# Performance work log

Hardware: AMD Instinct MI355X
Metric: run time of the kernel (lower is better)

The kernel has to match this reference:

```python
import jax, jax.numpy as jnp
import numpy as np

N = 20000
E = 320000
C = 16   # in_channels
G = 8    # growth_channels
H = 16   # kernel MLP hidden = RDB in_channels
DIM = 3
OMEGA = 100.0
BETA = 0.2


def _u(k, shape, s):
    return jax.random.uniform(k, shape, jnp.float32, -s, s)


def setup_inputs() -> dict:
    key = jax.random.key(0)
    ks = jax.random.split(key, 64)
    x = jax.random.normal(ks[0], (N, C), jnp.float32)
    pos = jax.random.normal(ks[1], (N, DIM), jnp.float32)
    # random edges with no self loops (add_remaining_self_loops appends them in reference)
    src = jax.random.randint(ks[2], (E,), 0, N)
    off = jax.random.randint(ks[3], (E,), 1, N)
    dst = (src + off) % N
    edge_index = jnp.stack([src, dst])
    d = {"x": x, "edge_index": edge_index, "pos": pos}
    ins = [C, C + G, C + 2 * G]
    outs = [G, G, C]
    i = 4
    for ci, (cin, cout) in enumerate(zip(ins, outs), 1):
        # SineLayer weights: uniform(-1/in_features, 1/in_features); biases ~ torch Linear default
        d[f"c{ci}_w0"] = _u(ks[i], (H, DIM + 1), 1.0 / (DIM + 1)); i += 1
        d[f"c{ci}_b0"] = _u(ks[i], (H,), 1.0 / np.sqrt(DIM + 1)); i += 1
        d[f"c{ci}_w1"] = _u(ks[i], (H, H), 1.0 / H); i += 1
        d[f"c{ci}_b1"] = _u(ks[i], (H,), 1.0 / np.sqrt(H)); i += 1
        d[f"c{ci}_w2"] = _u(ks[i], (H, H), 1.0 / H); i += 1
        d[f"c{ci}_b2"] = _u(ks[i], (H,), 1.0 / np.sqrt(H)); i += 1
        # final Linear(hidden -> in_size), stored transposed as [in_size, hidden]
        d[f"c{ci}_wl"] = _u(ks[i], (cin, H), 1.0 / np.sqrt(H)); i += 1
        d[f"c{ci}_bl"] = _u(ks[i], (cin,), 1.0 / np.sqrt(H)); i += 1
        d[f"c{ci}_bias"] = jnp.zeros((1, cout), jnp.float32); i += 1
    return d


def _edge_feat(pos, src, dst):
    # rel_pos = pos[dst] - pos[src]; spherical (rho, theta/pi, phi/pi), NaN at rho=0 -> 0
    rel = pos[dst] - pos[src]                              # [E,3]
    sq = jnp.sum(rel * rel, axis=1)
    zero = sq <= 0.0                                       # self loops
    rho = jnp.where(zero, 0.0, jnp.sqrt(jnp.where(zero, 1.0, sq)))
    theta = jnp.arctan2(jnp.where(zero, 0.0, rel[:, 1]), jnp.where(zero, 1.0, rel[:, 0]))
    phi = jnp.arcsin(jnp.clip(jnp.where(zero, 0.0, rel[:, 2]) / jnp.where(zero, 1.0, rho), -1.0, 1.0))
    return jnp.stack([rho, theta / jnp.pi, phi / jnp.pi], axis=1)  # [E,3]


def _gconv(feat, x, src, dst, n, out_ch, w0, b0, w1, b1, w2, b2, wl, bl, bias):
    # vectorized over output channels: channel index c is the 4th input of sin0
    base = feat @ w0[:, :3].T + b0                          # [E,H]
    ch = jnp.arange(out_ch, dtype=feat.dtype)               # [O]
    h = jnp.sin(OMEGA * (base[:, None, :] + ch[None, :, None] * w0[:, 3]))   # [E,O,H]
    h = jnp.sin(OMEGA * (jnp.einsum('eoh,gh->eog', h, w1) + b1))
    h = jnp.sin(OMEGA * (jnp.einsum('eoh,gh->eog', h, w2) + b2))
    xj = x[src]                                             # [E,in]
    # msg[e,o] = (Wl h[e,o] + bl) . x_j[e]  ==  h[e,o] . (Wl^T x_j[e]) + bl . x_j[e]
    msg = jnp.einsum('eoh,eh->eo', h, xj @ wl) + (xj @ bl)[:, None]
    return jax.ops.segment_sum(msg, dst, num_segments=n) + bias


def reference(x, edge_index, pos,
              c1_w0, c1_b0, c1_w1, c1_b1, c1_w2, c1_b2, c1_wl, c1_bl, c1_bias,
              c2_w0, c2_b0, c2_w1, c2_b1, c2_w2, c2_b2, c2_wl, c2_bl, c2_bias,
              c3_w0, c3_b0, c3_w1, c3_b1, c3_w2, c3_b2, c3_wl, c3_bl, c3_bias):
    n = x.shape[0]
    loop = jnp.arange(n, dtype=edge_index.dtype)
    src = jnp.concatenate([edge_index[0], loop])
    dst = jnp.concatenate([edge_index[1], loop])
    feat = _edge_feat(pos, src, dst)
    x1 = jax.nn.selu(_gconv(feat, x, src, dst, n, G, c1_w0, c1_b0, c1_w1, c1_b1, c1_w2, c1_b2, c1_wl, c1_bl, c1_bias))
    x2 = jax.nn.selu(_gconv(feat, jnp.concatenate([x, x1], 1), src, dst, n, G, c2_w0, c2_b0, c2_w1, c2_b1, c2_w2, c2_b2, c2_wl, c2_bl, c2_bias))
    x3 = jax.nn.selu(_gconv(feat, jnp.concatenate([x, x1, x2], 1), src, dst, n, C, c3_w0, c3_b0, c3_w1, c3_b1, c3_w2, c3_b2, c3_wl, c3_bl, c3_bias))
    return x + BETA * x3
```

## Files before the change

kernel.cpp:

```cpp
#include <hip/hip_runtime.h>
#include <math.h>

#define N_NODES 20000
#define N_EDGES 320000
#define HID 16
#define OMEGA 100.0f
#define BETA 0.2f
#define REVC 0.15915494309189535f

#define OFF_W0I 0
#define OFF_B1  64
#define OFF_B2  80
#define OFF_A2  128
#define OFF_WLH 384
#define OFF_WLL 640
#define OFF_AO  896
#define OFF_H2V 9088
#define P_SIZE  9472

typedef float  f32x4 __attribute__((ext_vector_type(4)));
typedef short  s16x8 __attribute__((ext_vector_type(8)));

__device__ __forceinline__ float sinrev(float x) { return __builtin_amdgcn_sinf(x); }
__device__ __forceinline__ float cosrev(float x) { return __builtin_amdgcn_cosf(x); }
__device__ __forceinline__ float fract_f(float x) { return __builtin_amdgcn_fractf(x); }

__device__ __forceinline__ float selu_f(float v) {
    const float a  = 1.6732632423543772f;
    const float sc = 1.0507009873554805f;
    return sc * (v > 0.f ? v : a * expm1f(v));
}

__device__ __forceinline__ f32x4 mfma16(s16x8 a, s16x8 b, f32x4 c) {
    return __builtin_amdgcn_mfma_f32_16x16x32_bf16(a, b, c, 0, 0, 0);
}

__device__ __forceinline__ unsigned pk_hi(float a, float b) {
    return (__float_as_uint(b) & 0xFFFF0000u) | (__float_as_uint(a) >> 16);
}
__device__ __forceinline__ float lo_of(float a) {
    return a - __uint_as_float(__float_as_uint(a) & 0xFFFF0000u);
}

union U4 { uint4 v; s16x8 s; };

struct PrepArgs {
    const float* w0[3]; const float* b0[3]; const float* w1[3]; const float* b1[3];
    const float* w2[3]; const float* b2[3]; const float* wl[3];
    float* P[3];
};

__global__ __launch_bounds__(256) void prep_kernel(PrepArgs A)
{
    const int INS[3]  = {16, 24, 32};
    const int OUTS[3] = {8, 8, 16};
    int c = blockIdx.x;
    int IN = INS[c], OUT = OUTS[c];
    const float* w0 = A.w0[c]; const float* b0 = A.b0[c];
    const float* w1 = A.w1[c]; const float* b1 = A.b1[c];
    const float* w2 = A.w2[c]; const float* b2 = A.b2[c];
    const float* wl = A.wl[c];
    float* P = A.P[c];
    unsigned* Pu = (unsigned*)P;

    __shared__ float W1s[256], W2s[256], cosB[256], sinB[256], w0c[16];
    int t = threadIdx.x;
    const float s = OMEGA * REVC;
    W1s[t] = s * w1[t];
    W2s[t] = s * w2[t];
    if (t < 16) w0c[t] = s * w0[t * 4 + 3];
    __syncthreads();

    if (t < 64) { int h = t >> 2, k = t & 3; P[t] = (k < 3) ? s * w0[h * 4 + k] : s * b0[h]; }
    if (t >= 64 && t < 80)  P[t] = s * b1[t - 64];
    if (t >= 80 && t < 96)  P[t] = s * b2[t - 80];

    if (t < OUT * 16) {
        int o = t >> 4, h = t & 15;
        float ang = fract_f((float)o * w0c[h]);
        cosB[t] = cosrev(ang);
        sinB[t] = sinrev(ang);
    }
    __syncthreads();

    if (t < 64) {
        int g = t & 15, q = t >> 4;
        float w[4], l[4];
#pragma unroll
        for (int j = 0; j < 4; j++) { w[j] = W2s[g * 16 + 4 * q + j]; l[j] = lo_of(w[j]); }
        ((uint4*)(Pu + OFF_A2))[t] = make_uint4(pk_hi(w[0], w[1]), pk_hi(w[2], w[3]),
                                                pk_hi(l[0], l[1]), pk_hi(l[2], l[3]));
    }
    if (t >= 64 && t < 128) {
        int lane = t - 64, g = lane & 15, q = lane >> 4;
        float v[8], l[8];
#pragma unroll
        for (int e = 0; e < 8; e++) {
            int i = 8 * q + e;
            v[e] = (i < IN) ? wl[i * 16 + g] : 0.f;
            l[e] = lo_of(v[e]);
        }
        ((uint4*)(Pu + OFF_WLH))[lane] = make_uint4(pk_hi(v[0], v[1]), pk_hi(v[2], v[3]),
                                                    pk_hi(v[4], v[5]), pk_hi(v[6], v[7]));
        ((uint4*)(Pu + OFF_WLL))[lane] = make_uint4(pk_hi(l[0], l[1]), pk_hi(l[2], l[3]),
                                                    pk_hi(l[4], l[5]), pk_hi(l[6], l[7]));
    }
    for (int idx = t; idx < OUT * 64; idx += 256) {
        int o = idx >> 6, lane = idx & 63, g = lane & 15, q = lane >> 4;
        float v[8], l[8];
#pragma unroll
        for (int e = 0; e < 8; e++) {
            int k = 8 * q + e;
            float a = (k < 16) ? W1s[g * 16 + k] * cosB[o * 16 + k]
                               : W1s[g * 16 + (k - 16)] * sinB[o * 16 + (k - 16)];
            v[e] = a; l[e] = lo_of(a);
        }
        ((uint4*)(Pu + OFF_AO + o * 512))[lane] =
            make_uint4(pk_hi(v[0], v[1]), pk_hi(v[2], v[3]), pk_hi(v[4], v[5]), pk_hi(v[6], v[7]));
        ((uint4*)(Pu + OFF_AO + o * 512 + 256))[lane] =
            make_uint4(pk_hi(l[0], l[1]), pk_hi(l[2], l[3]), pk_hi(l[4], l[5]), pk_hi(l[6], l[7]));
    }
    if (t < OUT) {
        float oc = (float)t;
        float h0[HID], h1[HID];
#pragma unroll
        for (int h = 0; h < HID; h++)
            h0[h] = sinrev(fract_f(fmaf(oc, w0c[h], s * b0[h])));
#pragma unroll
        for (int g = 0; g < HID; g++) {
            float sa = s * b1[g];
#pragma unroll
            for (int h = 0; h < HID; h++) sa += h0[h] * W1s[g * HID + h];
            h1[g] = sinrev(sa);
        }
#pragma unroll
        for (int g = 0; g < HID; g++) {
            float sa = s * b2[g];
#pragma unroll
            for (int h = 0; h < HID; h++) sa += h1[h] * W2s[g * HID + h];
            P[OFF_H2V + t * HID + g] = sinrev(sa);
        }
    }
}

__global__ __launch_bounds__(256) void fused_pre_kernel(
    const int* __restrict__ ei, const float* __restrict__ pos,
    const float* __restrict__ x,
    float4* __restrict__ feat, float* __restrict__ xcat,
    const float* __restrict__ wl1, const float* __restrict__ bl1,
    float* __restrict__ tb, float* __restrict__ blxb)
{
    int b = blockIdx.x;
    if (b < 1250) {
        int e = b * 256 + threadIdx.x;
        if (e >= N_EDGES) return;
        int s = ei[e], d = ei[N_EDGES + e];
        float rx = pos[d * 3 + 0] - pos[s * 3 + 0];
        float ry = pos[d * 3 + 1] - pos[s * 3 + 1];
        float rz = pos[d * 3 + 2] - pos[s * 3 + 2];
        float sq = rx * rx + ry * ry + rz * rz;
        float4 f = make_float4(0.f, 0.f, 0.f, 0.f);
        if (sq > 0.f) {
            float rho = sqrtf(sq);
            float th  = atan2f(ry, rx);
            float ph  = asinf(fminf(fmaxf(rz / rho, -1.f), 1.f));
            const float inv_pi = 0.31830988618379067f;
            f = make_float4(rho, th * inv_pi, ph * inv_pi, 0.f);
        }
        feat[e] = f;
    } else if (b < 2500) {
        int i = (b - 1250) * 256 + threadIdx.x;
        if (i >= N_NODES * 16) return;
        int n = i >> 4, cc = i & 15;
        xcat[n * 32 + cc] = x[i];
    } else {
        int n = (b - 2500) * 256 + threadIdx.x;
        if (n >= N_NODES) return;
        float tn[HID];
#pragma unroll
        for (int h = 0; h < HID; h++) tn[h] = 0.f;
        float bx = 0.f;
#pragma unroll
        for (int i = 0; i < 16; i++) {
            float xi = x[n * 16 + i];
            bx += bl1[i] * xi;
#pragma unroll
            for (int h = 0; h < HID; h++) tn[h] += wl1[i * 16 + h] * xi;
        }
#pragma unroll
        for (int h = 0; h < HID; h++) tb[n * 16 + h] = tn[h];
        blxb[n] = bx;
    }
}

template<int OUT, int IN>
__global__ __launch_bounds__(256) void conv_kernel(
    const int* __restrict__ ei, const float4* __restrict__ feat,
    const float* __restrict__ xcat, const float* __restrict__ P,
    const float* __restrict__ bl, float* __restrict__ acc)
{
    constexpr int L2O = (OUT == 16) ? 4 : 3;
    constexpr int EPI = 64 / OUT;
    constexpr int NI  = 16 / EPI;

    __shared__ float sm[4][OUT * 4 * 17];
    const unsigned* Pu = (const unsigned*)P;
    int wslot = threadIdx.x >> 6;
    int wid  = (blockIdx.x * 256 + threadIdx.x) >> 6;
    int lane = threadIdx.x & 63;
    int e16 = lane & 15, q = lane >> 4;
    int e = wid * 16 + e16;
    int src = ei[e];
    int dst = ei[N_EDGES + e];
    float4 f = feat[e];

    float tr[8];
    {
        const float4* w0i = (const float4*)P;
        int hb = (q & 1) * 8;
#pragma unroll
        for (int j = 0; j < 8; j++) {
            float4 w = w0i[hb + j];
            float ang = fract_f(w.w + f.x * w.x + f.y * w.y + f.z * w.z);
            tr[j] = (q < 2) ? sinrev(ang) : cosrev(ang);
        }
    }
    U4 Bh, Bl;
    Bh.v = make_uint4(pk_hi(tr[0], tr[1]), pk_hi(tr[2], tr[3]),
                      pk_hi(tr[4], tr[5]), pk_hi(tr[6], tr[7]));
    Bl.v = make_uint4(pk_hi(lo_of(tr[0]), lo_of(tr[1])), pk_hi(lo_of(tr[2]), lo_of(tr[3])),
                      pk_hi(lo_of(tr[4]), lo_of(tr[5])), pk_hi(lo_of(tr[6]), lo_of(tr[7])));

    float xv[8];
#pragma unroll
    for (int j = 0; j < 8; j++) xv[j] = 0.f;
    if (8 * q < IN) {
        const f32x4* xr = (const f32x4*)(xcat + src * 32 + 8 * q);
        f32x4 x0 = xr[0], x1 = xr[1];
        xv[0] = x0[0]; xv[1] = x0[1]; xv[2] = x0[2]; xv[3] = x0[3];
        xv[4] = x1[0]; xv[5] = x1[1]; xv[6] = x1[2]; xv[7] = x1[3];
    }
    U4 Xh, Xl;
    Xh.v = make_uint4(pk_hi(xv[0], xv[1]), pk_hi(xv[2], xv[3]),
                      pk_hi(xv[4], xv[5]), pk_hi(xv[6], xv[7]));
    Xl.v = make_uint4(pk_hi(lo_of(xv[0]), lo_of(xv[1])), pk_hi(lo_of(xv[2]), lo_of(xv[3])),
                      pk_hi(lo_of(xv[4]), lo_of(xv[5])), pk_hi(lo_of(xv[6]), lo_of(xv[7])));
    U4 WLh, WLl;
    WLh.v = ((const uint4*)(Pu + OFF_WLH))[lane];
    WLl.v = ((const uint4*)(Pu + OFF_WLL))[lane];
    f32x4 T = {0.f, 0.f, 0.f, 0.f};
    T = mfma16(WLh.s, Xh.s, T);
    T = mfma16(WLh.s, Xl.s, T);
    T = mfma16(WLl.s, Xh.s, T);

    float bx = 0.f;
    if (8 * q < IN) {
        const f32x4* blr = (const f32x4*)(bl + 8 * q);
        f32x4 b0v = blr[0], b1v = blr[1];
        bx = b0v[0] * xv[0] + b0v[1] * xv[1] + b0v[2] * xv[2] + b0v[3] * xv[3]
           + b1v[0] * xv[4] + b1v[1] * xv[5] + b1v[2] * xv[6] + b1v[3] * xv[7];
    }
    bx += __shfl_xor(bx, 16);
    bx += __shfl_xor(bx, 32);

    U4 A2; A2.v = ((const uint4*)(Pu + OFF_A2))[lane];
    f32x4 c1 = *(const f32x4*)(P + OFF_B1 + 4 * q);
    f32x4 c2 = *(const f32x4*)(P + OFF_B2 + 4 * q);

#pragma unroll 2
    for (int o = 0; o < OUT; ++o) {
        U4 Ah, Al;
        Ah.v = ((const uint4*)(Pu + OFF_AO + o * 512))[lane];
        Al.v = ((const uint4*)(Pu + OFF_AO + o * 512 + 256))[lane];
        f32x4 D = c1;
        D = mfma16(Ah.s, Bh.s, D);
        D = mfma16(Ah.s, Bl.s, D);
        D = mfma16(Al.s, Bh.s, D);
        float h1[4];
#pragma unroll
        for (int j = 0; j < 4; j++) h1[j] = sinrev(D[j]);
        unsigned p0 = pk_hi(h1[0], h1[1]), p1 = pk_hi(h1[2], h1[3]);
        unsigned l0 = pk_hi(lo_of(h1[0]), lo_of(h1[1])), l1 = pk_hi(lo_of(h1[2]), lo_of(h1[3]));
        U4 Ph, Pl;
        Ph.v = make_uint4(p0, p1, p0, p1);
        Pl.v = make_uint4(l0, l1, l0, l1);
        f32x4 D2 = c2;
        D2 = mfma16(A2.s, Ph.s, D2);
        D2 = mfma16(A2.s, Pl.s, D2);
        float p = sinrev(D2[0]) * T[0] + sinrev(D2[1]) * T[1]
                + sinrev(D2[2]) * T[2] + sinrev(D2[3]) * T[3];
        if (q == 0) p += bx;
        sm[wslot][(o * 4 + q) * 17 + e16] = p;
    }

    int oo = lane & (OUT - 1);
    int el = lane >> L2O;
#pragma unroll
    for (int j = 0; j < NI; j++) {
        int ej = j * EPI + el;
        int dj = __shfl(dst, ej);
        float v = sm[wslot][(oo * 4 + 0) * 17 + ej] + sm[wslot][(oo * 4 + 1) * 17 + ej]
                + sm[wslot][(oo * 4 + 2) * 17 + ej] + sm[wslot][(oo * 4 + 3) * 17 + ej];
        atomicAdd(&acc[dj * OUT + oo], v);
    }
}

template<int OUT, int CO>
__global__ __launch_bounds__(256) void finish_mid_kernel(
    const float* __restrict__ acc, const float* __restrict__ bias,
    const float* __restrict__ h2v,
    float* __restrict__ tb, float* __restrict__ blxb,
    float* __restrict__ xcat,
    const float* __restrict__ wlN, const float* __restrict__ blN)
{
    int n = blockIdx.x * 256 + threadIdx.x;
    if (n >= N_NODES) return;
    float trr[HID];
#pragma unroll
    for (int h = 0; h < HID; h++) trr[h] = tb[n * 16 + h];
    float bx = blxb[n];
    float xrow[CO + OUT];
#pragma unroll
    for (int i = 0; i < CO; i++) xrow[i] = xcat[n * 32 + i];
#pragma unroll
    for (int o = 0; o < OUT; o++) {
        float m = bx;
#pragma unroll
        for (int h = 0; h < HID; h++) m += h2v[o * 16 + h] * trr[h];
        float v = selu_f(acc[n * OUT + o] + bias[o] + m);
        xrow[CO + o] = v;
        xcat[n * 32 + CO + o] = v;
    }
    float tn[HID];
#pragma unroll
    for (int h = 0; h < HID; h++) tn[h] = 0.f;
    float bxn = 0.f;
#pragma unroll
    for (int i = 0; i < CO + OUT; i++) {
        float xi = xrow[i];
        bxn += blN[i] * xi;
#pragma unroll
        for (int h = 0; h < HID; h++) tn[h] += wlN[i * 16 + h] * xi;
    }
#pragma unroll
    for (int h = 0; h < HID; h++) tb[n * 16 + h] = tn[h];
    blxb[n] = bxn;
}

__global__ __launch_bounds__(256) void finish_out_kernel(
    const float* __restrict__ acc, const float* __restrict__ bias,
    const float* __restrict__ h2v,
    const float* __restrict__ tb, const float* __restrict__ blxb,
    const float* __restrict__ x, float* __restrict__ out)
{
    int n = blockIdx.x * 256 + threadIdx.x;
    if (n >= N_NODES) return;
    float trr[HID];
#pragma unroll
    for (int h = 0; h < HID; h++) trr[h] = tb[n * 16 + h];
    float bx = blxb[n];
#pragma unroll
    for (int c = 0; c < 16; c++) {
        float m = bx;
#pragma unroll
        for (int h = 0; h < HID; h++) m += h2v[c * 16 + h] * trr[h];
        out[n * 16 + c] = x[n * 16 + c] + BETA * selu_f(acc[n * 16 + c] + bias[c] + m);
    }
}

extern "C" void kernel_launch(void* const* d_in, const int* in_sizes, int n_in,
                              void* d_out, int out_size, void* d_ws, size_t ws_size,
                              hipStream_t stream)
{
    const float* x   = (const float*)d_in[0];
    const int*   ei  = (const int*)d_in[1];
    const float* pos = (const float*)d_in[2];

    const float* W[27];
    for (int i = 0; i < 27; i++) W[i] = (const float*)d_in[3 + i];

    float* ws    = (float*)d_ws;
    float4* feat = (float4*)ws;
    float* xcat  = ws + (size_t)N_EDGES * 4;
    float* acc1  = xcat + (size_t)N_NODES * 32;
    float* acc2  = acc1 + (size_t)N_NODES * 8;
    float* acc3  = acc2 + (size_t)N_NODES * 8;
    float* P1    = acc3 + (size_t)N_NODES * 16;
    float* P2    = P1 + P_SIZE;
    float* P3    = P2 + P_SIZE;
    float* tb    = P3 + P_SIZE;
    float* blxb  = tb + (size_t)N_NODES * 16;
    float* out   = (float*)d_out;

    hipMemsetAsync(acc1, 0, (size_t)N_NODES * 32 * sizeof(float), stream);

    PrepArgs pa;
    for (int c = 0; c < 3; c++) {
        pa.w0[c] = W[9 * c + 0]; pa.b0[c] = W[9 * c + 1];
        pa.w1[c] = W[9 * c + 2]; pa.b1[c] = W[9 * c + 3];
        pa.w2[c] = W[9 * c + 4]; pa.b2[c] = W[9 * c + 5];
        pa.wl[c] = W[9 * c + 6];
    }
    pa.P[0] = P1; pa.P[1] = P2; pa.P[2] = P3;

    dim3 blk(256);
    prep_kernel<<<3, blk, 0, stream>>>(pa);
    fused_pre_kernel<<<2579, blk, 0, stream>>>(ei, pos, x, feat, xcat, W[6], W[7], tb, blxb);

    conv_kernel<8, 16><<<5000, blk, 0, stream>>>(ei, feat, xcat, P1, W[7], acc1);
    finish_mid_kernel<8, 16><<<79, blk, 0, stream>>>(acc1, W[8], P1 + OFF_H2V, tb, blxb, xcat, W[15], W[16]);

    conv_kernel<8, 24><<<5000, blk, 0, stream>>>(ei, feat, xcat, P2, W[16], acc2);
    finish_mid_kernel<8, 24><<<79, blk, 0, stream>>>(acc2, W[17], P2 + OFF_H2V, tb, blxb, xcat, W[24], W[25]);

    conv_kernel<16, 32><<<5000, blk, 0, stream>>>(ei, feat, xcat, P3, W[25], acc3);
    finish_out_kernel<<<79, blk, 0, stream>>>(acc3, W[26], P3 + OFF_H2V, tb, blxb, x, out);
}
```

Baseline: 180.5 us.

## Precompute per-node Wl^T x and bl·x once instead of per edge

```diff
diff --git a/kernel.cpp b/kernel.cpp
--- a/kernel.cpp
+++ b/kernel.cpp
@@ -12,8 +12,6 @@
 #define OFF_B1  64
 #define OFF_B2  80
 #define OFF_A2  128
-#define OFF_WLH 384
-#define OFF_WLL 640
 #define OFF_AO  896
 #define OFF_H2V 9088
 #define P_SIZE  9472
@@ -46,20 +44,18 @@
 
 struct PrepArgs {
     const float* w0[3]; const float* b0[3]; const float* w1[3]; const float* b1[3];
-    const float* w2[3]; const float* b2[3]; const float* wl[3];
+    const float* w2[3]; const float* b2[3];
     float* P[3];
 };
 
 __global__ __launch_bounds__(256) void prep_kernel(PrepArgs A)
 {
-    const int INS[3]  = {16, 24, 32};
     const int OUTS[3] = {8, 8, 16};
     int c = blockIdx.x;
-    int IN = INS[c], OUT = OUTS[c];
+    int OUT = OUTS[c];
     const float* w0 = A.w0[c]; const float* b0 = A.b0[c];
     const float* w1 = A.w1[c]; const float* b1 = A.b1[c];
     const float* w2 = A.w2[c]; const float* b2 = A.b2[c];
-    const float* wl = A.wl[c];
     float* P = A.P[c];
     unsigned* Pu = (unsigned*)P;
 
@@ -90,20 +86,6 @@
         for (int j = 0; j < 4; j++) { w[j] = W2s[g * 16 + 4 * q + j]; l[j] = lo_of(w[j]); }
         ((uint4*)(Pu + OFF_A2))[t] = make_uint4(pk_hi(w[0], w[1]), pk_hi(w[2], w[3]),
                                                 pk_hi(l[0], l[1]), pk_hi(l[2], l[3]));
-    }
-    if (t >= 64 && t < 128) {
-        int lane = t - 64, g = lane & 15, q = lane >> 4;
-        float v[8], l[8];
-#pragma unroll
-        for (int e = 0; e < 8; e++) {
-            int i = 8 * q + e;
-            v[e] = (i < IN) ? wl[i * 16 + g] : 0.f;
-            l[e] = lo_of(v[e]);
-        }
-        ((uint4*)(Pu + OFF_WLH))[lane] = make_uint4(pk_hi(v[0], v[1]), pk_hi(v[2], v[3]),
-                                                    pk_hi(v[4], v[5]), pk_hi(v[6], v[7]));
-        ((uint4*)(Pu + OFF_WLL))[lane] = make_uint4(pk_hi(l[0], l[1]), pk_hi(l[2], l[3]),
-                                                    pk_hi(l[4], l[5]), pk_hi(l[6], l[7]));
     }
     for (int idx = t; idx < OUT * 64; idx += 256) {
         int o = idx >> 6, lane = idx & 63, g = lane & 15, q = lane >> 4;
@@ -193,11 +175,11 @@
     }
 }
 
-template<int OUT, int IN>
+template<int OUT>
 __global__ __launch_bounds__(256) void conv_kernel(
     const int* __restrict__ ei, const float4* __restrict__ feat,
-    const float* __restrict__ xcat, const float* __restrict__ P,
-    const float* __restrict__ bl, float* __restrict__ acc)
+    const float* __restrict__ tbn, const float* __restrict__ blxn,
+    const float* __restrict__ P, float* __restrict__ acc)
 {
     constexpr int L2O = (OUT == 16) ? 4 : 3;
     constexpr int EPI = 64 / OUT;
@@ -214,6 +196,9 @@
     int dst = ei[N_EDGES + e];
     float4 f = feat[e];
 
+    f32x4 T = *(const f32x4*)(tbn + src * 16 + 4 * q);
+    float bx = blxn[src];
+
     float tr[8];
     {
         const float4* w0i = (const float4*)P;
@@ -230,38 +215,6 @@
                       pk_hi(tr[4], tr[5]), pk_hi(tr[6], tr[7]));
     Bl.v = make_uint4(pk_hi(lo_of(tr[0]), lo_of(tr[1])), pk_hi(lo_of(tr[2]), lo_of(tr[3])),
                       pk_hi(lo_of(tr[4]), lo_of(tr[5])), pk_hi(lo_of(tr[6]), lo_of(tr[7])));
-
-    float xv[8];
-#pragma unroll
-    for (int j = 0; j < 8; j++) xv[j] = 0.f;
-    if (8 * q < IN) {
-        const f32x4* xr = (const f32x4*)(xcat + src * 32 + 8 * q);
-        f32x4 x0 = xr[0], x1 = xr[1];
-        xv[0] = x0[0]; xv[1] = x0[1]; xv[2] = x0[2]; xv[3] = x0[3];
-        xv[4] = x1[0]; xv[5] = x1[1]; xv[6] = x1[2]; xv[7] = x1[3];
-    }
-    U4 Xh, Xl;
-    Xh.v = make_uint4(pk_hi(xv[0], xv[1]), pk_hi(xv[2], xv[3]),
-                      pk_hi(xv[4], xv[5]), pk_hi(xv[6], xv[7]));
-    Xl.v = make_uint4(pk_hi(lo_of(xv[0]), lo_of(xv[1])), pk_hi(lo_of(xv[2]), lo_of(xv[3])),
-                      pk_hi(lo_of(xv[4]), lo_of(xv[5])), pk_hi(lo_of(xv[6]), lo_of(xv[7])));
-    U4 WLh, WLl;
-    WLh.v = ((const uint4*)(Pu + OFF_WLH))[lane];
-    WLl.v = ((const uint4*)(Pu + OFF_WLL))[lane];
-    f32x4 T = {0.f, 0.f, 0.f, 0.f};
-    T = mfma16(WLh.s, Xh.s, T);
-    T = mfma16(WLh.s, Xl.s, T);
-    T = mfma16(WLl.s, Xh.s, T);
-
-    float bx = 0.f;
-    if (8 * q < IN) {
-        const f32x4* blr = (const f32x4*)(bl + 8 * q);
-        f32x4 b0v = blr[0], b1v = blr[1];
-        bx = b0v[0] * xv[0] + b0v[1] * xv[1] + b0v[2] * xv[2] + b0v[3] * xv[3]
-           + b1v[0] * xv[4] + b1v[1] * xv[5] + b1v[2] * xv[6] + b1v[3] * xv[7];
-    }
-    bx += __shfl_xor(bx, 16);
-    bx += __shfl_xor(bx, 32);
 
     U4 A2; A2.v = ((const uint4*)(Pu + OFF_A2))[lane];
     f32x4 c1 = *(const f32x4*)(P + OFF_B1 + 4 * q);
@@ -399,7 +352,6 @@
         pa.w0[c] = W[9 * c + 0]; pa.b0[c] = W[9 * c + 1];
         pa.w1[c] = W[9 * c + 2]; pa.b1[c] = W[9 * c + 3];
         pa.w2[c] = W[9 * c + 4]; pa.b2[c] = W[9 * c + 5];
-        pa.wl[c] = W[9 * c + 6];
     }
     pa.P[0] = P1; pa.P[1] = P2; pa.P[2] = P3;
 
@@ -407,12 +359,12 @@
     prep_kernel<<<3, blk, 0, stream>>>(pa);
     fused_pre_kernel<<<2579, blk, 0, stream>>>(ei, pos, x, feat, xcat, W[6], W[7], tb, blxb);
 
-    conv_kernel<8, 16><<<5000, blk, 0, stream>>>(ei, feat, xcat, P1, W[7], acc1);
+    conv_kernel<8><<<5000, blk, 0, stream>>>(ei, feat, tb, blxb, P1, acc1);
     finish_mid_kernel<8, 16><<<79, blk, 0, stream>>>(acc1, W[8], P1 + OFF_H2V, tb, blxb, xcat, W[15], W[16]);
 
-    conv_kernel<8, 24><<<5000, blk, 0, stream>>>(ei, feat, xcat, P2, W[16], acc2);
+    conv_kernel<8><<<5000, blk, 0, stream>>>(ei, feat, tb, blxb, P2, acc2);
     finish_mid_kernel<8, 24><<<79, blk, 0, stream>>>(acc2, W[17], P2 + OFF_H2V, tb, blxb, xcat, W[24], W[25]);
 
-    conv_kernel<16, 32><<<5000, blk, 0, stream>>>(ei, feat, xcat, P3, W[25], acc3);
+    conv_kernel<16><<<5000, blk, 0, stream>>>(ei, feat, tb, blxb, P3, acc3);
     finish_out_kernel<<<79, blk, 0, stream>>>(acc3, W[26], P3 + OFF_H2V, tb, blxb, x, out);
 }
```

Result: faster. 167.5 us (-7.2%).
